# Kernel optimization log

Hardware: AMD Instinct MI355X
Metric: run time of the kernel (lower is better)

Reference implementation:

```python
import jax, jax.numpy as jnp
import numpy as np

B, S, H = 4, 1024, 1024
NH = 16
DH = H // NH  # 64


def setup_inputs() -> dict:
    key = jax.random.key(0)
    ks = jax.random.split(key, 8)
    std = 1.0 / np.sqrt(H)
    return {
        "query": jax.random.normal(ks[0], (B, S, H), jnp.float32),
        "key": jax.random.normal(ks[1], (B, S, H), jnp.float32),
        "value": jax.random.normal(ks[2], (B, S, H), jnp.float32),
        "masks": jnp.ones((B, S), jnp.float32),
        "Wq": jax.random.normal(ks[3], (H, H), jnp.float32) * std,
        "bq": jnp.zeros((H,), jnp.float32),
        "Wk": jax.random.normal(ks[4], (H, H), jnp.float32) * std,
        "bk": jnp.zeros((H,), jnp.float32),
        "Wv": jax.random.normal(ks[5], (H, H), jnp.float32) * std,
        "bv": jnp.zeros((H,), jnp.float32),
    }


def reference(query, key, value, masks, Wq, bq, Wk, bk, Wv, bv):
    # ReLU-gated projections (torch Linear: x @ W.T + b)
    qp = jax.nn.relu(jnp.einsum("bsh,oh->bso", query, Wq) + bq)
    kp = jax.nn.relu(jnp.einsum("bsh,oh->bso", key, Wk) + bk)
    vp = jax.nn.relu(jnp.einsum("bsh,oh->bso", value, Wv) + bv)
    # chunk(dim=2)+cat(dim=0) == split hidden into (NH, DH) contiguous slices
    qh = qp.reshape(B, S, NH, DH)
    kh = kp.reshape(B, S, NH, DH)
    vh = vp.reshape(B, S, NH, DH)
    scale = 1.0 / jnp.sqrt(jnp.asarray(DH, qp.dtype))
    # [B, NH, Sq, Sk]
    alpha = jnp.einsum("bqnd,bknd->bnqk", qh, kh) * scale
    alpha = jax.nn.softmax(alpha, axis=-1)
    # post-softmax multiplicative mask, applied per QUERY position
    alpha = alpha * masks[:, None, :, None]
    hiddens = jnp.einsum("bnqk,bknd->bqnd", alpha, vh).reshape(B, S, H)
    return hiddens + query
```

## Files before the change

### kernel.cpp

```cpp
#include <hip/hip_runtime.h>


typedef __attribute__((ext_vector_type(8))) __bf16 bf16x8;
typedef __attribute__((ext_vector_type(4))) float f32x4;
typedef __attribute__((ext_vector_type(16))) float f32x16;
typedef __attribute__((ext_vector_type(8))) unsigned short u16x8;
typedef __attribute__((ext_vector_type(4))) unsigned short u16x4;

#define XQ_OFF 0u
#define XK_OFF 4194304u
#define XV_OFF 8388608u
#define WQ_OFF 12582912u
#define WK_OFF 13631488u
#define WV_OFF 14680064u
#define QP_OFF 15728640u
#define KP_OFF 19922944u
#define VT_OFF 24117248u

__device__ __forceinline__ unsigned short f2bf(float f) {
  union { float f; unsigned int u; } c; c.f = f;
  return (unsigned short)((c.u + 0x7fffu + ((c.u >> 16) & 1u)) >> 16);
}

__global__ __launch_bounds__(256) void cvt_kernel(
    const float* __restrict__ q, const float* __restrict__ k, const float* __restrict__ v,
    const float* __restrict__ wq, const float* __restrict__ wk, const float* __restrict__ wv,
    unsigned short* __restrict__ ws) {
  const int z = blockIdx.y;
  const float* src; unsigned short* dst; int n;
  switch (z) {
    case 0: src = q;  dst = ws + XQ_OFF; n = 4194304; break;
    case 1: src = k;  dst = ws + XK_OFF; n = 4194304; break;
    case 2: src = v;  dst = ws + XV_OFF; n = 4194304; break;
    case 3: src = wq; dst = ws + WQ_OFF; n = 1048576; break;
    case 4: src = wk; dst = ws + WK_OFF; n = 1048576; break;
    default: src = wv; dst = ws + WV_OFF; n = 1048576; break;
  }
  const int i8 = (blockIdx.x * 256 + threadIdx.x) * 8;
  if (i8 >= n) return;
  const float4 f0 = *(const float4*)(src + i8);
  const float4 f1 = *(const float4*)(src + i8 + 4);
  u16x8 r;
  r[0] = f2bf(f0.x); r[1] = f2bf(f0.y); r[2] = f2bf(f0.z); r[3] = f2bf(f0.w);
  r[4] = f2bf(f1.x); r[5] = f2bf(f1.y); r[6] = f2bf(f1.z); r[7] = f2bf(f1.w);
  *(u16x8*)(dst + i8) = r;
}

__global__ __launch_bounds__(256) void proj_gemm(
    unsigned short* __restrict__ ws,
    const float* __restrict__ bq, const float* __restrict__ bk, const float* __restrict__ bv) {
  __shared__ unsigned short smem[18432];
  const int z = blockIdx.z;
  const unsigned short* X = ws + (z == 0 ? XQ_OFF : z == 1 ? XK_OFF : XV_OFF);
  const unsigned short* W = ws + (z == 0 ? WQ_OFF : z == 1 ? WK_OFF : WV_OFF);
  unsigned short* P = ws + (z == 0 ? QP_OFF : z == 1 ? KP_OFF : VT_OFF);
  const float* bias = z == 0 ? bq : z == 1 ? bk : bv;

  const int tid  = threadIdx.x;
  const int lane = tid & 63;
  const int w    = tid >> 6;
  const int l31  = lane & 31;
  const int g    = lane >> 5;
  const int wr = w >> 1, wc = w & 1;

  const int lin = blockIdx.x + 8 * blockIdx.y;
  const int xcd = lin & 7;
  const int idx = lin >> 3;
  const int m0 = (xcd * 4 + (idx >> 3)) * 128;
  const int n0 = (idx & 7) * 128;

  f32x16 acc[2][2];
#pragma unroll
  for (int i = 0; i < 2; ++i)
#pragma unroll
    for (int j = 0; j < 2; ++j)
#pragma unroll
      for (int r = 0; r < 16; ++r) acc[i][j][r] = 0.f;

  const int c1 = 256 + tid;
  const int row0 = tid >> 2, kc0 = (((tid & 3) ^ (row0 & 3)) * 8);
  const int row1 = c1 >> 2,  kc1 = (((c1 & 3) ^ (row1 & 3)) * 8);
  const unsigned short* gA0 = X + (size_t)(m0 + row0) * 1024 + kc0;
  const unsigned short* gA1 = X + (size_t)(m0 + row1) * 1024 + kc1;
  const unsigned short* gB0 = W + (size_t)(n0 + row0) * 1024 + kc0;
  const unsigned short* gB1 = W + (size_t)(n0 + row1) * 1024 + kc1;
  const int d0 = w * 512, d1 = 2048 + w * 512;

  auto stage = [&](int buf) {
    unsigned short* Ab = smem + buf * 8192;
    unsigned short* Bb = Ab + 4096;
    __builtin_amdgcn_global_load_lds((const __attribute__((address_space(1))) void*)gA0,
                                     (__attribute__((address_space(3))) void*)(Ab + d0), 16, 0, 0);
    __builtin_amdgcn_global_load_lds((const __attribute__((address_space(1))) void*)gB0,
                                     (__attribute__((address_space(3))) void*)(Bb + d0), 16, 0, 0);
    __builtin_amdgcn_global_load_lds((const __attribute__((address_space(1))) void*)gA1,
                                     (__attribute__((address_space(3))) void*)(Ab + d1), 16, 0, 0);
    __builtin_amdgcn_global_load_lds((const __attribute__((address_space(1))) void*)gB1,
                                     (__attribute__((address_space(3))) void*)(Bb + d1), 16, 0, 0);
    gA0 += 32; gA1 += 32; gB0 += 32; gB1 += 32;
  };
  auto compute = [&](int buf) {
    const unsigned short* Ab = smem + buf * 8192;
    const unsigned short* Bb = Ab + 4096;
    bf16x8 af[2][2], bfv[2][2];
#pragma unroll
    for (int mt = 0; mt < 2; ++mt)
#pragma unroll
      for (int kk = 0; kk < 2; ++kk) {
        const int ra = wr * 64 + mt * 32 + l31;
        af[mt][kk] = *(const bf16x8*)&Ab[ra * 32 + (((kk * 2 + g) ^ (ra & 3)) * 8)];
      }
#pragma unroll
    for (int nt = 0; nt < 2; ++nt)
#pragma unroll
      for (int kk = 0; kk < 2; ++kk) {
        const int rb = wc * 64 + nt * 32 + l31;
        bfv[nt][kk] = *(const bf16x8*)&Bb[rb * 32 + (((kk * 2 + g) ^ (rb & 3)) * 8)];
      }
#pragma unroll
    for (int mt = 0; mt < 2; ++mt)
#pragma unroll
      for (int nt = 0; nt < 2; ++nt)
#pragma unroll
        for (int kk = 0; kk < 2; ++kk)
          acc[mt][nt] = __builtin_amdgcn_mfma_f32_32x32x16_bf16(af[mt][kk], bfv[nt][kk],
                                                                acc[mt][nt], 0, 0, 0);
  };

  stage(0);
  for (int kt = 0; kt < 32; kt += 2) {
    __syncthreads();
    stage(1);
    compute(0);
    __syncthreads();
    if (kt != 30) stage(0);
    compute(1);
  }
  __syncthreads();

  unsigned short* Tw = smem + w * 4608;
  if (z != 2) {
#pragma unroll
    for (int mt = 0; mt < 2; ++mt)
#pragma unroll
      for (int nt = 0; nt < 2; ++nt) {
        const float bvv = bias[n0 + wc * 64 + nt * 32 + l31];
#pragma unroll
        for (int reg = 0; reg < 16; ++reg) {
          const int rloc = (reg & 3) + 8 * (reg >> 2) + 4 * g;
          float v = acc[mt][nt][reg] + bvv;
          v = v > 0.f ? v : 0.f;
          Tw[(mt * 32 + rloc) * 72 + nt * 32 + l31] = f2bf(v);
        }
      }
    const int row0g = m0 + wr * 64;
    const int colb  = n0 + wc * 64;
#pragma unroll
    for (int i = 0; i < 8; ++i) {
      const int rr = i * 8 + (lane >> 3);
      const int cc = (lane & 7) * 8;
      *(u16x8*)&P[(size_t)(row0g + rr) * 1024 + colb + cc] = *(const u16x8*)&Tw[rr * 72 + cc];
    }
  } else {
#pragma unroll
    for (int mt = 0; mt < 2; ++mt)
#pragma unroll
      for (int nt = 0; nt < 2; ++nt) {
        const float bvv = bias[n0 + wc * 64 + nt * 32 + l31];
#pragma unroll
        for (int rq = 0; rq < 4; ++rq) {
          u16x4 pk;
#pragma unroll
          for (int r = 0; r < 4; ++r) {
            float v = acc[mt][nt][rq * 4 + r] + bvv;
            v = v > 0.f ? v : 0.f;
            pk[r] = f2bf(v);
          }
          *(u16x4*)&Tw[(nt * 32 + l31) * 72 + mt * 32 + rq * 8 + g * 4] = pk;
        }
      }
    const int h2 = (n0 >> 6) + wc;
    const int bb = m0 >> 10;
    const int s0 = (m0 & 1023) + wr * 64;
#pragma unroll
    for (int i = 0; i < 8; ++i) {
      const int rr = i * 8 + (lane >> 3);
      const int cc = (lane & 7) * 8;
      *(u16x8*)&P[((size_t)(bb * 16 + h2) * 64 + rr) * 1024 + s0 + cc] =
          *(const u16x8*)&Tw[rr * 72 + cc];
    }
  }
}

__global__ __launch_bounds__(256) void attn_kernel(
    const unsigned short* __restrict__ QP, const unsigned short* __restrict__ KP,
    const unsigned short* __restrict__ VT, const float* __restrict__ masks,
    const float* __restrict__ query, float* __restrict__ out) {
  __shared__ unsigned short Kt[2][64 * 64];
  __shared__ unsigned short Vt[2][64 * 64];
  __shared__ unsigned short Pl[4][32 * 72];
  const int tid  = threadIdx.x;
  const int lane = tid & 63;
  const int w    = tid >> 6;
  const int quad = lane >> 4;
  const int l15  = lane & 15;
  const int bh = blockIdx.x;
  const int b = bh >> 4, h = bh & 15;
  const int q0w = blockIdx.y * 128 + w * 32;
  const size_t base = (size_t)b * 1024 * 1024;

  bf16x8 qf[2][2];
#pragma unroll
  for (int mt = 0; mt < 2; ++mt)
#pragma unroll
    for (int kk = 0; kk < 2; ++kk)
      qf[mt][kk] = *(const bf16x8*)&QP[base + (size_t)(q0w + mt * 16 + l15) * 1024 +
                                       h * 64 + kk * 32 + quad * 8];

  f32x4 o[2][4];
  float lsum[2] = {0.f, 0.f};
#pragma unroll
  for (int mt = 0; mt < 2; ++mt)
#pragma unroll
    for (int nd = 0; nd < 4; ++nd) o[mt][nd] = f32x4{0.f, 0.f, 0.f, 0.f};

  const int r_st = lane >> 3;
  const int pc   = lane & 7;
  const int swz  = l15 & 7;
  const float cvt = 0.18033688011112042f;

  auto stage = [&](int key0, int buf) {
#pragma unroll
    for (int t = 0; t < 2; ++t) {
      const int rowk = (w * 2 + t) * 8 + r_st;
      const int lc   = pc ^ (rowk & 7);
      const unsigned short* gk = &KP[base + (size_t)(key0 + rowk) * 1024 + h * 64 + lc * 8];
      const unsigned short* gv = &VT[((size_t)bh * 64 + rowk) * 1024 + key0 + lc * 8];
      __builtin_amdgcn_global_load_lds((const __attribute__((address_space(1))) void*)gk,
                                       (__attribute__((address_space(3))) void*)&Kt[buf][(w * 2 + t) * 512],
                                       16, 0, 0);
      __builtin_amdgcn_global_load_lds((const __attribute__((address_space(1))) void*)gv,
                                       (__attribute__((address_space(3))) void*)&Vt[buf][(w * 2 + t) * 512],
                                       16, 0, 0);
    }
  };

  stage(0, 0);
  for (int kb = 0; kb < 16; ++kb) {
    __syncthreads();
    if (kb < 15) stage((kb + 1) * 64, (kb + 1) & 1);
    const unsigned short* Ktb = Kt[kb & 1];
    const unsigned short* Vtb = Vt[kb & 1];

    bf16x8 kf[2][4];
#pragma unroll
    for (int kk = 0; kk < 2; ++kk)
#pragma unroll
      for (int ni = 0; ni < 4; ++ni)
        kf[kk][ni] = *(const bf16x8*)&Ktb[(ni * 16 + l15) * 64 + ((kk * 4 + quad) ^ swz) * 8];

#pragma unroll
    for (int mt = 0; mt < 2; ++mt) {
      f32x4 st[4];
#pragma unroll
      for (int ni = 0; ni < 4; ++ni) st[ni] = f32x4{0.f, 0.f, 0.f, 0.f};
#pragma unroll
      for (int kk = 0; kk < 2; ++kk)
#pragma unroll
        for (int ni = 0; ni < 4; ++ni)
          st[ni] = __builtin_amdgcn_mfma_f32_16x16x32_bf16(kf[kk][ni], qf[mt][kk], st[ni], 0, 0, 0);
      float ls = 0.f;
#pragma unroll
      for (int ni = 0; ni < 4; ++ni) {
        float p0 = exp2f(fmaf(st[ni][0], cvt, -8.0f));
        float p1 = exp2f(fmaf(st[ni][1], cvt, -8.0f));
        float p2 = exp2f(fmaf(st[ni][2], cvt, -8.0f));
        float p3 = exp2f(fmaf(st[ni][3], cvt, -8.0f));
        ls += (p0 + p1) + (p2 + p3);
        const unsigned int u0 = __float_as_uint(p0) + 0x8000u;
        const unsigned int u1 = __float_as_uint(p1) + 0x8000u;
        const unsigned int u2 = __float_as_uint(p2) + 0x8000u;
        const unsigned int u3 = __float_as_uint(p3) + 0x8000u;
        uint2 pk;
        pk.x = (u0 >> 16) | (u1 & 0xffff0000u);
        pk.y = (u2 >> 16) | (u3 & 0xffff0000u);
        *(uint2*)&Pl[w][(mt * 16 + l15) * 72 + ni * 16 + quad * 4] = pk;
      }
      lsum[mt] += ls;
    }

#pragma unroll
    for (int kk = 0; kk < 2; ++kk) {
      bf16x8 pa[2];
#pragma unroll
      for (int mt = 0; mt < 2; ++mt)
        pa[mt] = *(const bf16x8*)&Pl[w][(mt * 16 + l15) * 72 + kk * 32 + quad * 8];
#pragma unroll
      for (int nd = 0; nd < 4; ++nd) {
        bf16x8 vf = *(const bf16x8*)&Vtb[(nd * 16 + l15) * 64 + ((kk * 4 + quad) ^ swz) * 8];
#pragma unroll
        for (int mt = 0; mt < 2; ++mt)
          o[mt][nd] = __builtin_amdgcn_mfma_f32_16x16x32_bf16(pa[mt], vf, o[mt][nd], 0, 0, 0);
      }
    }
  }

#pragma unroll
  for (int mt = 0; mt < 2; ++mt) {
    lsum[mt] += __shfl_xor(lsum[mt], 16);
    lsum[mt] += __shfl_xor(lsum[mt], 32);
  }

#pragma unroll
  for (int mt = 0; mt < 2; ++mt)
#pragma unroll
    for (int r = 0; r < 4; ++r) {
      const int rq = quad * 4 + r;
      const float ls = __shfl(lsum[mt], (lane & 48) | rq);
      const int row = q0w + mt * 16 + rq;
      const float scale = masks[b * 1024 + row] / ls;
#pragma unroll
      for (int nd = 0; nd < 4; ++nd) {
        const int col = h * 64 + nd * 16 + l15;
        const size_t gi = base + (size_t)row * 1024 + col;
        out[gi] = o[mt][nd][r] * scale + query[gi];
      }
    }
}

extern "C" void kernel_launch(void* const* d_in, const int* in_sizes, int n_in,
                              void* d_out, int out_size, void* d_ws, size_t ws_size,
                              hipStream_t stream) {
  const float* q     = (const float*)d_in[0];
  const float* k     = (const float*)d_in[1];
  const float* v     = (const float*)d_in[2];
  const float* masks = (const float*)d_in[3];
  const float* Wq    = (const float*)d_in[4];
  const float* bq    = (const float*)d_in[5];
  const float* Wk    = (const float*)d_in[6];
  const float* bk    = (const float*)d_in[7];
  const float* Wv    = (const float*)d_in[8];
  const float* bv    = (const float*)d_in[9];
  float* out = (float*)d_out;
  unsigned short* ws = (unsigned short*)d_ws;

  cvt_kernel<<<dim3(2048, 6), 256, 0, stream>>>(q, k, v, Wq, Wk, Wv, ws);
  proj_gemm<<<dim3(8, 32, 3), 256, 0, stream>>>(ws, bq, bk, bv);
  attn_kernel<<<dim3(64, 8), 256, 0, stream>>>(ws + QP_OFF, ws + KP_OFF, ws + VT_OFF,
                                               masks, q, out);
}
```

Before: 197.5 us.

## Deepen projection GEMM to 4-stage LDS pipeline with vmcnt waits and new swizzle

The projection GEMM moves from a double-buffered loop with two full __syncthreads per iteration to a 4-buffer ring. Each iteration waits only for the oldest global_load_lds batch, using s_waitcnt vmcnt(8) plus a single s_barrier, so more tile loads stay in flight while MFMAs run. The LDS XOR swizzle now keys on (row>>1)&3 to cut bank conflicts on the bf16x8 fragment reads. s_setprio raises wave priority around the MFMA block. LDS per block grows to 64KB, which may reduce how many blocks fit per CU.

```diff
diff --git a/kernel.cpp b/kernel.cpp
--- a/kernel.cpp
+++ b/kernel.cpp
@@ -49,7 +49,7 @@
 __global__ __launch_bounds__(256) void proj_gemm(
     unsigned short* __restrict__ ws,
     const float* __restrict__ bq, const float* __restrict__ bk, const float* __restrict__ bv) {
-  __shared__ unsigned short smem[18432];
+  __shared__ unsigned short smem[32768];
   const int z = blockIdx.z;
   const unsigned short* X = ws + (z == 0 ? XQ_OFF : z == 1 ? XK_OFF : XV_OFF);
   const unsigned short* W = ws + (z == 0 ? WQ_OFF : z == 1 ? WK_OFF : WV_OFF);
@@ -78,8 +78,8 @@
       for (int r = 0; r < 16; ++r) acc[i][j][r] = 0.f;
 
   const int c1 = 256 + tid;
-  const int row0 = tid >> 2, kc0 = (((tid & 3) ^ (row0 & 3)) * 8);
-  const int row1 = c1 >> 2,  kc1 = (((c1 & 3) ^ (row1 & 3)) * 8);
+  const int row0 = tid >> 2, kc0 = (((tid & 3) ^ ((row0 >> 1) & 3)) * 8);
+  const int row1 = c1 >> 2,  kc1 = (((c1 & 3) ^ ((row1 >> 1) & 3)) * 8);
   const unsigned short* gA0 = X + (size_t)(m0 + row0) * 1024 + kc0;
   const unsigned short* gA1 = X + (size_t)(m0 + row1) * 1024 + kc1;
   const unsigned short* gB0 = W + (size_t)(n0 + row0) * 1024 + kc0;
@@ -108,15 +108,16 @@
 #pragma unroll
       for (int kk = 0; kk < 2; ++kk) {
         const int ra = wr * 64 + mt * 32 + l31;
-        af[mt][kk] = *(const bf16x8*)&Ab[ra * 32 + (((kk * 2 + g) ^ (ra & 3)) * 8)];
+        af[mt][kk] = *(const bf16x8*)&Ab[ra * 32 + (((kk * 2 + g) ^ ((ra >> 1) & 3)) * 8)];
       }
 #pragma unroll
     for (int nt = 0; nt < 2; ++nt)
 #pragma unroll
       for (int kk = 0; kk < 2; ++kk) {
         const int rb = wc * 64 + nt * 32 + l31;
-        bfv[nt][kk] = *(const bf16x8*)&Bb[rb * 32 + (((kk * 2 + g) ^ (rb & 3)) * 8)];
-      }
+        bfv[nt][kk] = *(const bf16x8*)&Bb[rb * 32 + (((kk * 2 + g) ^ ((rb >> 1) & 3)) * 8)];
+      }
+    __builtin_amdgcn_s_setprio(1);
 #pragma unroll
     for (int mt = 0; mt < 2; ++mt)
 #pragma unroll
@@ -125,18 +126,25 @@
         for (int kk = 0; kk < 2; ++kk)
           acc[mt][nt] = __builtin_amdgcn_mfma_f32_32x32x16_bf16(af[mt][kk], bfv[nt][kk],
                                                                 acc[mt][nt], 0, 0, 0);
+    __builtin_amdgcn_s_setprio(0);
   };
 
-  stage(0);
-  for (int kt = 0; kt < 32; kt += 2) {
-    __syncthreads();
-    stage(1);
-    compute(0);
-    __syncthreads();
-    if (kt != 30) stage(0);
-    compute(1);
-  }
-  __syncthreads();
+  stage(0); stage(1); stage(2);
+  for (int t = 0; t < 29; ++t) {
+    asm volatile("s_waitcnt vmcnt(8)" ::: "memory");
+    __builtin_amdgcn_s_barrier();
+    stage((t + 3) & 3);
+    compute(t & 3);
+  }
+  asm volatile("s_waitcnt vmcnt(8)" ::: "memory");
+  __builtin_amdgcn_s_barrier();
+  compute(1);
+  asm volatile("s_waitcnt vmcnt(4)" ::: "memory");
+  __builtin_amdgcn_s_barrier();
+  compute(2);
+  asm volatile("s_waitcnt vmcnt(0)" ::: "memory");
+  __builtin_amdgcn_s_barrier();
+  compute(3);
 
   unsigned short* Tw = smem + w * 4608;
   if (z != 2) {
```

Result: faster. 184.9 us (-6.4%).
